# Kernel tuning notes

Measured on AMD Instinct MI355X. Metric: run time of the kernel, lower is better.

Reference implementation:

```python
import jax, jax.numpy as jnp
import numpy as np

N = 51200      # total nodes
E = 1638400    # total edges (avg degree 32)
G = 512        # graphs in batch
IN = 16        # input node features
H = 4          # heads
C = 32         # channels per head
HC = H * C     # 128, concat output width
SLOPE = 0.2    # LeakyReLU negative slope
BN_EPS = 1e-5


def _glorot(k, shape, fan):
    return jax.random.normal(k, shape, jnp.float32) / np.sqrt(fan).astype(np.float32)


def setup_inputs() -> dict:
    key = jax.random.key(0)
    ks = jax.random.split(key, 32)
    inp = {}
    inp['x'] = jax.random.normal(ks[0], (N, IN), jnp.float32)
    inp['edge_index'] = jax.random.randint(ks[1], (2, E), 0, N)
    inp['batch'] = jnp.sort(jax.random.randint(ks[2], (N,), 0, G))
    # GATv2 layer 1 (IN -> H*C)
    inp['l1_Wl'] = _glorot(ks[3], (IN, HC), IN)
    inp['l1_bl'] = jnp.zeros((HC,), jnp.float32)
    inp['l1_Wr'] = _glorot(ks[4], (IN, HC), IN)
    inp['l1_br'] = jnp.zeros((HC,), jnp.float32)
    inp['l1_att'] = _glorot(ks[5], (H, C), C)
    inp['l1_bias'] = jnp.zeros((HC,), jnp.float32)
    # GATv2 layer 2 (HC -> H*C)
    inp['l2_Wl'] = _glorot(ks[6], (HC, HC), HC)
    inp['l2_bl'] = jnp.zeros((HC,), jnp.float32)
    inp['l2_Wr'] = _glorot(ks[7], (HC, HC), HC)
    inp['l2_br'] = jnp.zeros((HC,), jnp.float32)
    inp['l2_att'] = _glorot(ks[8], (H, C), C)
    inp['l2_bias'] = jnp.zeros((HC,), jnp.float32)
    # MLP head (HC -> HC -> HC -> 2) with BatchNorm (eval mode, running stats 0/1)
    inp['fc1_W'] = _glorot(ks[9], (HC, HC), HC)
    inp['fc1_b'] = jnp.zeros((HC,), jnp.float32)
    inp['bn1_g'] = jnp.ones((HC,), jnp.float32)
    inp['bn1_b'] = jnp.zeros((HC,), jnp.float32)
    inp['fc2_W'] = _glorot(ks[10], (HC, HC), HC)
    inp['fc2_b'] = jnp.zeros((HC,), jnp.float32)
    inp['bn2_g'] = jnp.ones((HC,), jnp.float32)
    inp['bn2_b'] = jnp.zeros((HC,), jnp.float32)
    inp['fc3_W'] = _glorot(ks[11], (HC, 2), HC)
    inp['fc3_b'] = jnp.zeros((2,), jnp.float32)
    return inp


def gatv2_conv(x, src, dst, Wl, bl, Wr, br, att, bias):
    # PyG GATv2Conv (share_weights=False, concat=True), eval mode (no dropout).
    xl = (x @ Wl + bl).reshape(-1, H, C)  # source transform  [N,H,C]
    xr = (x @ Wr + br).reshape(-1, H, C)  # target transform  [N,H,C]
    e = jax.nn.leaky_relu(xl[src] + xr[dst], SLOPE)   # [E,H,C]
    score = jnp.einsum('ehc,hc->eh', e, att)          # [E,H]
    # segment softmax over edges sharing the same target node
    m = jax.ops.segment_max(score, dst, num_segments=N)
    ex = jnp.exp(score - m[dst])
    denom = jax.ops.segment_sum(ex, dst, num_segments=N)
    alpha = ex / (denom[dst] + 1e-16)                 # [E,H]
    out = jax.ops.segment_sum(xl[src] * alpha[:, :, None], dst, num_segments=N)
    return out.reshape(-1, HC) + bias


def reference(x, edge_index, batch,
              l1_Wl, l1_bl, l1_Wr, l1_br, l1_att, l1_bias,
              l2_Wl, l2_bl, l2_Wr, l2_br, l2_att, l2_bias,
              fc1_W, fc1_b, bn1_g, bn1_b,
              fc2_W, fc2_b, bn2_g, bn2_b,
              fc3_W, fc3_b):
    src, dst = edge_index[0], edge_index[1]
    h = jax.nn.relu(gatv2_conv(x, src, dst, l1_Wl, l1_bl, l1_Wr, l1_br, l1_att, l1_bias))
    h = jax.nn.relu(gatv2_conv(h, src, dst, l2_Wl, l2_bl, l2_Wr, l2_br, l2_att, l2_bias))
    # global mean pool over graphs
    s = jax.ops.segment_sum(h, batch, num_segments=G)
    cnt = jax.ops.segment_sum(jnp.ones((N,), h.dtype), batch, num_segments=G)
    g = s / jnp.maximum(cnt, 1.0)[:, None]            # [G,HC]
    # MLP head; BatchNorm1d in eval mode with running_mean=0, running_var=1
    def bn(z, gamma, beta):
        return z * (gamma / np.sqrt(1.0 + BN_EPS).astype(np.float32)) + beta
    g = jax.nn.relu(bn(g @ fc1_W + fc1_b, bn1_g, bn1_b))
    g = jax.nn.relu(bn(g @ fc2_W + fc2_b, bn2_g, bn2_b))
    return g @ fc3_W + fc3_b                          # [G,2]
```

## Files before the change

kernel.cpp:

```cpp
#include <hip/hip_runtime.h>
#include <math.h>

#define NN 51200
#define EE 1638400
#define GG 512
#define INF 16
#define HCC 128
#define NB 400
#define TILE 4096

typedef float vf2 __attribute__((ext_vector_type(2)));
#define FMA2 __builtin_elementwise_fma
#define MIN2 __builtin_elementwise_min
#define MAX2 __builtin_elementwise_max


__global__ __launch_bounds__(256) void k_hist(const int* __restrict__ ei,
                                              int* __restrict__ bcnt) {
    __shared__ int h[NB];
    for (int i = threadIdx.x; i < NB; i += 256) h[i] = 0;
    __syncthreads();
    int e0 = blockIdx.x * TILE;
#pragma unroll
    for (int s = 0; s < 16; s++) {
        int d = ei[EE + e0 + s * 256 + threadIdx.x];
        atomicAdd(&h[d >> 7], 1);
    }
    __syncthreads();
    for (int i = threadIdx.x; i < NB; i += 256)
        if (h[i]) atomicAdd(&bcnt[i], h[i]);
}

__global__ __launch_bounds__(512) void k_scan2(const int* __restrict__ bcnt,
                                               int* __restrict__ bbase,
                                               int* __restrict__ gcur,
                                               int* __restrict__ rowptr) {
    __shared__ int sc[512];
    int t = threadIdx.x;
    int v = (t < NB) ? bcnt[t] : 0;
    sc[t] = v;
    __syncthreads();
    for (int off = 1; off < 512; off <<= 1) {
        int u = (t >= off) ? sc[t - off] : 0;
        __syncthreads();
        sc[t] += u;
        __syncthreads();
    }
    if (t < NB) { int ex = sc[t] - v; bbase[t] = ex; gcur[t] = ex; }
    if (t == 0) { bbase[NB] = EE; rowptr[NN] = EE; }
}

__global__ __launch_bounds__(512) void k_bin(const int* __restrict__ ei,
                                             int* __restrict__ gcur,
                                             unsigned* __restrict__ binned) {
    __shared__ int h[512];
    __shared__ int lexcl[NB], lcur[NB], baseg[NB];
    __shared__ unsigned stage[TILE];
    int t = threadIdx.x;
    h[t] = 0;
    __syncthreads();
    int e0 = blockIdx.x * TILE;
    int sv[8], dv[8];
#pragma unroll
    for (int s = 0; s < 8; s++) {
        int e = e0 + s * 512 + t;
        sv[s] = ei[e];
        dv[s] = ei[EE + e];
        atomicAdd(&h[dv[s] >> 7], 1);
    }
    __syncthreads();
    int myh = h[t];
    for (int off = 1; off < 512; off <<= 1) {
        int u = (t >= off) ? h[t - off] : 0;
        __syncthreads();
        h[t] += u;
        __syncthreads();
    }
    if (t < NB) {
        int ex = h[t] - myh;
        lexcl[t] = ex;
        lcur[t] = ex;
        baseg[t] = atomicAdd(&gcur[t], myh);
    }
    __syncthreads();
#pragma unroll
    for (int s = 0; s < 8; s++) {
        int b = dv[s] >> 7;
        int r = atomicAdd(&lcur[b], 1);
        stage[r] = (unsigned)sv[s] | ((unsigned)dv[s] << 16);
    }
    __syncthreads();
#pragma unroll
    for (int s = 0; s < 8; s++) {
        int idx = s * 512 + t;
        unsigned p = stage[idx];
        int b = (int)(p >> 23);
        binned[baseg[b] + idx - lexcl[b]] = p;
    }
}

__global__ __launch_bounds__(256) void k_csr(const unsigned* __restrict__ binned,
                                             const int* __restrict__ bbase,
                                             int* __restrict__ rowptr,
                                             int* __restrict__ col) {
    int b = blockIdx.x;
    int base = bbase[b];
    int cnt = bbase[b + 1] - base;
    __shared__ int nh[128], ncur[128];
    int t = threadIdx.x;
    if (t < 128) nh[t] = 0;
    __syncthreads();
    for (int e = t; e < cnt; e += 256) {
        unsigned p = binned[base + e];
        atomicAdd(&nh[(p >> 16) & 127], 1);
    }
    __syncthreads();
    int myv = (t < 128) ? nh[t] : 0;
    for (int off = 1; off < 128; off <<= 1) {
        int u = (t >= off && t < 128) ? nh[t - off] : 0;
        __syncthreads();
        if (t < 128) nh[t] += u;
        __syncthreads();
    }
    if (t < 128) {
        int ex = nh[t] - myv;
        rowptr[(b << 7) + t] = base + ex;
        ncur[t] = base + ex;
    }
    __syncthreads();
    for (int e = t; e < cnt; e += 256) {
        unsigned p = binned[base + e];
        int r = atomicAdd(&ncur[(p >> 16) & 127], 1);
        col[r] = (int)(p & 0xFFFFu);
    }
}

__global__ __launch_bounds__(256) void k_lin1(const float* __restrict__ x,
                                              const float* __restrict__ Wl,
                                              const float* __restrict__ bl,
                                              const float* __restrict__ Wr,
                                              const float* __restrict__ br,
                                              float* __restrict__ xl,
                                              float* __restrict__ xr) {
    __shared__ float sx[2][INF];
    int j = threadIdx.x & 127;
    int ty = threadIdx.x >> 7;
    int row = blockIdx.x * 2 + ty;
    if (threadIdx.x < 32) {
        int r = blockIdx.x * 2 + (threadIdx.x >> 4);
        sx[threadIdx.x >> 4][threadIdx.x & 15] = x[(size_t)r * INF + (threadIdx.x & 15)];
    }
    __syncthreads();
    float al = bl[j], ar = br[j];
#pragma unroll
    for (int k = 0; k < INF; k++) {
        float xv = sx[ty][k];
        al = fmaf(xv, Wl[k * HCC + j], al);
        ar = fmaf(xv, Wr[k * HCC + j], ar);
    }
    int s = 64 * ((j >> 2) & 1) + 4 * (j >> 3) + (j & 3);
    xl[(size_t)row * HCC + s] = al;
    xr[(size_t)row * HCC + s] = ar;
}

#define AST 129
#define BST 260
__global__ __launch_bounds__(512) void k_lin2(const float* __restrict__ hin,
                                              const float* __restrict__ Wl,
                                              const float* __restrict__ bl,
                                              const float* __restrict__ Wr,
                                              const float* __restrict__ br,
                                              float* __restrict__ outl,
                                              float* __restrict__ outr) {
    __shared__ float As[32 * AST];
    __shared__ float Bs[32 * BST];
    const int tid = threadIdx.x;
    const int cx = tid & 31;
    const int cy = tid >> 5;
    const int r0 = blockIdx.x * 128;

    float accL[8][4], accR[8][4];
#pragma unroll
    for (int j = 0; j < 8; j++)
#pragma unroll
        for (int i = 0; i < 4; i++) { accL[j][i] = 0.f; accR[j][i] = 0.f; }

    for (int k0 = 0; k0 < HCC; k0 += 32) {
#pragma unroll
        for (int s = 0; s < 2; s++) {
            int f = tid + 512 * s;
            int row = f >> 3;
            int kk = (f & 7) * 4;
            float4 v = *(const float4*)(hin + (size_t)(r0 + row) * HCC + k0 + kk);
            As[(kk + 0) * AST + row] = v.x;
            As[(kk + 1) * AST + row] = v.y;
            As[(kk + 2) * AST + row] = v.z;
            As[(kk + 3) * AST + row] = v.w;
        }
#pragma unroll
        for (int s = 0; s < 4; s++) {
            int g = tid + 512 * s;
            int kr = g >> 6;
            int c4 = g & 63;
            const float* srcp = (c4 < 32)
                ? (Wl + (size_t)(k0 + kr) * HCC + c4 * 4)
                : (Wr + (size_t)(k0 + kr) * HCC + (c4 - 32) * 4);
            *(float4*)&Bs[kr * BST + c4 * 4] = *(const float4*)srcp;
        }
        __syncthreads();
#pragma unroll 4
        for (int k = 0; k < 32; ++k) {
            float a[8];
#pragma unroll
            for (int j = 0; j < 8; ++j) a[j] = As[k * AST + cy + 16 * j];
            float4 b4l = *(const float4*)&Bs[k * BST + cx * 4];
            float4 b4r = *(const float4*)&Bs[k * BST + 128 + cx * 4];
#pragma unroll
            for (int j = 0; j < 8; ++j) {
                accL[j][0] = fmaf(a[j], b4l.x, accL[j][0]);
                accL[j][1] = fmaf(a[j], b4l.y, accL[j][1]);
                accL[j][2] = fmaf(a[j], b4l.z, accL[j][2]);
                accL[j][3] = fmaf(a[j], b4l.w, accL[j][3]);
                accR[j][0] = fmaf(a[j], b4r.x, accR[j][0]);
                accR[j][1] = fmaf(a[j], b4r.y, accR[j][1]);
                accR[j][2] = fmaf(a[j], b4r.z, accR[j][2]);
                accR[j][3] = fmaf(a[j], b4r.w, accR[j][3]);
            }
        }
        __syncthreads();
    }
    float4 bv_l = *(const float4*)(bl + cx * 4);
    float4 bv_r = *(const float4*)(br + cx * 4);
    const int soff = 64 * (cx & 1) + (cx >> 1) * 4;
#pragma unroll
    for (int j = 0; j < 8; ++j) {
        int row = r0 + cy + 16 * j;
        float4 o;
        o.x = accL[j][0] + bv_l.x;
        o.y = accL[j][1] + bv_l.y;
        o.z = accL[j][2] + bv_l.z;
        o.w = accL[j][3] + bv_l.w;
        *(float4*)(outl + (size_t)row * HCC + soff) = o;
        o.x = accR[j][0] + bv_r.x;
        o.y = accR[j][1] + bv_r.y;
        o.z = accR[j][2] + bv_r.z;
        o.w = accR[j][3] + bv_r.w;
        *(float4*)(outr + (size_t)row * HCC + soff) = o;
    }
}

__global__ __launch_bounds__(256) void k_attn(const int* __restrict__ rowptr,
                                              const int* __restrict__ col,
                                              const float* __restrict__ xl,
                                              const float* __restrict__ xr,
                                              const float* __restrict__ att,
                                              const float* __restrict__ bias,
                                              float* __restrict__ hout) {
    const int wave = threadIdx.x >> 6;
    const int lane = threadIdx.x & 63;
    const int sub = lane >> 4;
    const int q = lane & 15;
    const int n = blockIdx.x * 4 + wave;

    const float4 xrv0 = *(const float4*)(xr + (size_t)n * HCC + q * 4);
    const float4 xrv1 = *(const float4*)(xr + (size_t)n * HCC + 64 + q * 4);
    const float4 at0 = *(const float4*)(att + q * 8);
    const float4 at1 = *(const float4*)(att + q * 8 + 4);
    const vf2 xr01 = {xrv0.x, xrv0.y}, xr23 = {xrv0.z, xrv0.w};
    const vf2 xr45 = {xrv1.x, xrv1.y}, xr67 = {xrv1.z, xrv1.w};
    const vf2 at01 = {at0.x, at0.y}, at23 = {at0.z, at0.w};
    const vf2 at45 = {at1.x, at1.y}, at67 = {at1.z, at1.w};
    const vf2 Z2 = {0.f, 0.f}, C2 = {0.2f, 0.2f};
    const unsigned choff = (unsigned)q * 16u;

    const int base = rowptr[n];
    const int deg = rowptr[n + 1] - base;

    float m = -INFINITY, l = 0.f;
    vf2 a01 = Z2, a23 = Z2, a45 = Z2, a67 = Z2;

    for (int i0 = 0; i0 < deg; i0 += 64) {
        int mye = 0;
        if (i0 + lane < deg) mye = col[base + i0 + lane];
        const int cnt = min(64, deg - i0);
        const int groups = (cnt + 15) >> 4;
        for (int g = 0; g < groups; ++g) {
            vf2 v01[4], v23[4], v45[4], v67[4];
#pragma unroll
            for (int k = 0; k < 4; ++k) {
                const int src = __shfl(mye, 16 * g + 4 * k + sub);
                const unsigned voff = ((unsigned)src << 9) + choff;
                const float4 v0 = *(const float4*)((const char*)xl + voff);
                const float4 v1 = *(const float4*)((const char*)xl + voff + 256);
                v01[k] = (vf2){v0.x, v0.y}; v23[k] = (vf2){v0.z, v0.w};
                v45[k] = (vf2){v1.x, v1.y}; v67[k] = (vf2){v1.z, v1.w};
            }
            float p[4];
#pragma unroll
            for (int k = 0; k < 4; ++k) {
                vf2 e, kk, p2;
                e = v01[k] + xr01; kk = FMA2(C2, MIN2(e, Z2), MAX2(e, Z2)); p2 = kk * at01;
                e = v23[k] + xr23; kk = FMA2(C2, MIN2(e, Z2), MAX2(e, Z2)); p2 = FMA2(kk, at23, p2);
                e = v45[k] + xr45; kk = FMA2(C2, MIN2(e, Z2), MAX2(e, Z2)); p2 = FMA2(kk, at45, p2);
                e = v67[k] + xr67; kk = FMA2(C2, MIN2(e, Z2), MAX2(e, Z2)); p2 = FMA2(kk, at67, p2);
                float pp = p2.x + p2.y;
                pp += __shfl_xor(pp, 1);
                pp += __shfl_xor(pp, 2);
                if ((16 * g + 4 * k + sub) >= cnt) pp = -INFINITY;
                p[k] = pp;
            }
            float pm = fmaxf(fmaxf(p[0], p[1]), fmaxf(p[2], p[3]));
            pm = fmaxf(pm, __shfl_xor(pm, 16));
            pm = fmaxf(pm, __shfl_xor(pm, 32));
            const float mn = fmaxf(m, pm);
            const float sc = __expf(m - mn);
            const float w0 = __expf(p[0] - mn);
            const float w1 = __expf(p[1] - mn);
            const float w2 = __expf(p[2] - mn);
            const float w3 = __expf(p[3] - mn);
            l = fmaf(l, sc, (w0 + w1) + (w2 + w3));
            const vf2 S = {sc, sc};
            const vf2 W0 = {w0, w0}, W1 = {w1, w1}, W2 = {w2, w2}, W3 = {w3, w3};
            a01 = FMA2(W3, v01[3], FMA2(W2, v01[2], FMA2(W1, v01[1], FMA2(W0, v01[0], a01 * S))));
            a23 = FMA2(W3, v23[3], FMA2(W2, v23[2], FMA2(W1, v23[1], FMA2(W0, v23[0], a23 * S))));
            a45 = FMA2(W3, v45[3], FMA2(W2, v45[2], FMA2(W1, v45[1], FMA2(W0, v45[0], a45 * S))));
            a67 = FMA2(W3, v67[3], FMA2(W2, v67[2], FMA2(W1, v67[1], FMA2(W0, v67[0], a67 * S))));
            m = mn;
        }
    }
    l += __shfl_xor(l, 16);
    l += __shfl_xor(l, 32);
    float af[8] = {a01.x, a01.y, a23.x, a23.y, a45.x, a45.y, a67.x, a67.y};
#pragma unroll
    for (int i = 0; i < 8; i++) {
        af[i] += __shfl_xor(af[i], 16);
        af[i] += __shfl_xor(af[i], 32);
    }
    const float inv = 1.f / (l + 1e-16f);
    if (sub == 0) {
        const float4 b0 = *(const float4*)(bias + q * 8);
        const float4 b1 = *(const float4*)(bias + q * 8 + 4);
        float4 o0, o1;
        o0.x = fmaxf(fmaf(af[0], inv, b0.x), 0.f);
        o0.y = fmaxf(fmaf(af[1], inv, b0.y), 0.f);
        o0.z = fmaxf(fmaf(af[2], inv, b0.z), 0.f);
        o0.w = fmaxf(fmaf(af[3], inv, b0.w), 0.f);
        o1.x = fmaxf(fmaf(af[4], inv, b1.x), 0.f);
        o1.y = fmaxf(fmaf(af[5], inv, b1.y), 0.f);
        o1.z = fmaxf(fmaf(af[6], inv, b1.z), 0.f);
        o1.w = fmaxf(fmaf(af[7], inv, b1.w), 0.f);
        *(float4*)(hout + (size_t)n * HCC + q * 8) = o0;
        *(float4*)(hout + (size_t)n * HCC + q * 8 + 4) = o1;
    }
}

__global__ __launch_bounds__(128) void k_head(const float* __restrict__ h,
                                              const int* __restrict__ batch,
                                              const float* __restrict__ fc1W, const float* __restrict__ fc1b,
                                              const float* __restrict__ bn1g, const float* __restrict__ bn1b,
                                              const float* __restrict__ fc2W, const float* __restrict__ fc2b,
                                              const float* __restrict__ bn2g, const float* __restrict__ bn2b,
                                              const float* __restrict__ fc3W, const float* __restrict__ fc3b,
                                              float* __restrict__ out) {
    int g = blockIdx.x;
    int j = threadIdx.x;
    __shared__ float buf[HCC], buf2[HCC];
    int lo = 0, hi = NN;
    while (lo < hi) { int mid = (lo + hi) >> 1; if (batch[mid] < g) lo = mid + 1; else hi = mid; }
    int s = lo;
    lo = 0; hi = NN;
    while (lo < hi) { int mid = (lo + hi) >> 1; if (batch[mid] < g + 1) lo = mid + 1; else hi = mid; }
    int e = lo;
    float sum = 0.f;
    for (int n = s; n < e; n++) sum += h[(size_t)n * HCC + j];
    float cnt = (float)(e - s);
    buf[j] = sum / fmaxf(cnt, 1.0f);
    __syncthreads();
    const float SQ = 1.00000499998749994f;
    float a = fc1b[j];
    for (int k = 0; k < HCC; k++) a = fmaf(buf[k], fc1W[k * HCC + j], a);
    a = fmaf(a, bn1g[j] / SQ, bn1b[j]);
    a = fmaxf(a, 0.f);
    buf2[j] = a;
    __syncthreads();
    a = fc2b[j];
    for (int k = 0; k < HCC; k++) a = fmaf(buf2[k], fc2W[k * HCC + j], a);
    a = fmaf(a, bn2g[j] / SQ, bn2b[j]);
    a = fmaxf(a, 0.f);
    buf[j] = a;
    __syncthreads();
    if (j < 2) {
        float o = fc3b[j];
        for (int k = 0; k < HCC; k++) o = fmaf(buf[k], fc3W[k * 2 + j], o);
        out[g * 2 + j] = o;
    }
}

extern "C" void kernel_launch(void* const* d_in, const int* in_sizes, int n_in,
                              void* d_out, int out_size, void* d_ws, size_t ws_size,
                              hipStream_t stream) {
    const float* x      = (const float*)d_in[0];
    const int*   ei     = (const int*)d_in[1];
    const int*   batch  = (const int*)d_in[2];
    const float* l1_Wl  = (const float*)d_in[3];
    const float* l1_bl  = (const float*)d_in[4];
    const float* l1_Wr  = (const float*)d_in[5];
    const float* l1_br  = (const float*)d_in[6];
    const float* l1_att = (const float*)d_in[7];
    const float* l1_bias= (const float*)d_in[8];
    const float* l2_Wl  = (const float*)d_in[9];
    const float* l2_bl  = (const float*)d_in[10];
    const float* l2_Wr  = (const float*)d_in[11];
    const float* l2_br  = (const float*)d_in[12];
    const float* l2_att = (const float*)d_in[13];
    const float* l2_bias= (const float*)d_in[14];
    const float* fc1_W  = (const float*)d_in[15];
    const float* fc1_b  = (const float*)d_in[16];
    const float* bn1_g  = (const float*)d_in[17];
    const float* bn1_b  = (const float*)d_in[18];
    const float* fc2_W  = (const float*)d_in[19];
    const float* fc2_b  = (const float*)d_in[20];
    const float* bn2_g  = (const float*)d_in[21];
    const float* bn2_b  = (const float*)d_in[22];
    const float* fc3_W  = (const float*)d_in[23];
    const float* fc3_b  = (const float*)d_in[24];
    float* out = (float*)d_out;

    float* xl = (float*)d_ws;
    float* xr = xl + (size_t)NN * HCC;
    float* h  = xr + (size_t)NN * HCC;
    int* rowptr = (int*)(h + (size_t)NN * HCC);
    int* col    = rowptr + (NN + 1);
    int* bcnt   = col + EE;
    int* bbase  = bcnt + NB;
    int* gcur   = bbase + (NB + 1);
    unsigned* binned = (unsigned*)xl;

    hipMemsetAsync(bcnt, 0, NB * sizeof(int), stream);
    k_hist<<<EE / TILE, 256, 0, stream>>>(ei, bcnt);
    k_scan2<<<1, 512, 0, stream>>>(bcnt, bbase, gcur, rowptr);
    k_bin<<<EE / TILE, 512, 0, stream>>>(ei, gcur, binned);
    k_csr<<<NB, 256, 0, stream>>>(binned, bbase, rowptr, col);

    k_lin1<<<NN / 2, 256, 0, stream>>>(x, l1_Wl, l1_bl, l1_Wr, l1_br, xl, xr);
    k_attn<<<NN / 4, 256, 0, stream>>>(rowptr, col, xl, xr, l1_att, l1_bias, h);

    k_lin2<<<NN / 128, 512, 0, stream>>>(h, l2_Wl, l2_bl, l2_Wr, l2_br, xl, xr);
    k_attn<<<NN / 4, 256, 0, stream>>>(rowptr, col, xl, xr, l2_att, l2_bias, h);

    k_head<<<GG, 128, 0, stream>>>(h, batch, fc1_W, fc1_b, bn1_g, bn1_b,
                                   fc2_W, fc2_b, bn2_g, bn2_b, fc3_W, fc3_b, out);
}
```

Before: 516.4 us.

## Sort CSR columns by source bucket and use wave-shuffle scans

The CSR build now partitions each destination row's edges into 8 buckets keyed by the top bits of the source index, so neighbor lists are roughly ordered by source. The aim is better cache locality for the later xl[src] gathers. The shared-memory Hillis-Steele scans in k_bin and k_csr are replaced by wave shuffle scans with per-wave sums, which cuts barrier count. The pooling loop in k_head is split into four accumulators for more memory-level parallelism, which changes the order of float summation.

```diff
diff --git a/kernel.cpp b/kernel.cpp
--- a/kernel.cpp
+++ b/kernel.cpp
@@ -14,6 +14,15 @@
 #define MIN2 __builtin_elementwise_min
 #define MAX2 __builtin_elementwise_max
 
+
+__device__ __forceinline__ int wave_incl_scan(int v, int lane) {
+#pragma unroll
+    for (int d = 1; d < 64; d <<= 1) {
+        int y = __shfl_up(v, d);
+        if (lane >= d) v += y;
+    }
+    return v;
+}
 
 __global__ __launch_bounds__(256) void k_hist(const int* __restrict__ ei,
                                               int* __restrict__ bcnt) {
@@ -56,7 +65,9 @@
     __shared__ int h[512];
     __shared__ int lexcl[NB], lcur[NB], baseg[NB];
     __shared__ unsigned stage[TILE];
+    __shared__ int wsum[8];
     int t = threadIdx.x;
+    int lane = t & 63, w = t >> 6;
     h[t] = 0;
     __syncthreads();
     int e0 = blockIdx.x * TILE;
@@ -70,14 +81,14 @@
     }
     __syncthreads();
     int myh = h[t];
-    for (int off = 1; off < 512; off <<= 1) {
-        int u = (t >= off) ? h[t - off] : 0;
-        __syncthreads();
-        h[t] += u;
-        __syncthreads();
-    }
+    int incl = wave_incl_scan(myh, lane);
+    if (lane == 63) wsum[w] = incl;
+    __syncthreads();
+    int woff = 0;
+    for (int i = 0; i < w; i++) woff += wsum[i];
+    incl += woff;
     if (t < NB) {
-        int ex = h[t] - myh;
+        int ex = incl - myh;
         lexcl[t] = ex;
         lcur[t] = ex;
         baseg[t] = atomicAdd(&gcur[t], myh);
@@ -106,32 +117,40 @@
     int b = blockIdx.x;
     int base = bbase[b];
     int cnt = bbase[b + 1] - base;
-    __shared__ int nh[128], ncur[128];
+    __shared__ int nh[1024], ncur[1024];
+    __shared__ int wsum[4];
     int t = threadIdx.x;
-    if (t < 128) nh[t] = 0;
+    int lane = t & 63, w = t >> 6;
+#pragma unroll
+    for (int i = 0; i < 4; i++) nh[t + 256 * i] = 0;
     __syncthreads();
     for (int e = t; e < cnt; e += 256) {
         unsigned p = binned[base + e];
-        atomicAdd(&nh[(p >> 16) & 127], 1);
-    }
-    __syncthreads();
-    int myv = (t < 128) ? nh[t] : 0;
-    for (int off = 1; off < 128; off <<= 1) {
-        int u = (t >= off && t < 128) ? nh[t - off] : 0;
-        __syncthreads();
-        if (t < 128) nh[t] += u;
-        __syncthreads();
-    }
-    if (t < 128) {
-        int ex = nh[t] - myv;
-        rowptr[(b << 7) + t] = base + ex;
-        ncur[t] = base + ex;
-    }
+        unsigned src = p & 0xFFFFu;
+        int key = (int)(((p >> 16) & 127u) << 3) | (int)(src >> 13);
+        atomicAdd(&nh[key], 1);
+    }
+    __syncthreads();
+    int c0 = nh[4 * t + 0], c1 = nh[4 * t + 1], c2 = nh[4 * t + 2], c3 = nh[4 * t + 3];
+    int tot = ((c0 + c1) + (c2 + c3));
+    int incl = wave_incl_scan(tot, lane);
+    if (lane == 63) wsum[w] = incl;
+    __syncthreads();
+    int woff = 0;
+    for (int i = 0; i < w; i++) woff += wsum[i];
+    int tex = incl + woff - tot;
+    ncur[4 * t + 0] = base + tex;
+    ncur[4 * t + 1] = base + tex + c0;
+    ncur[4 * t + 2] = base + tex + c0 + c1;
+    ncur[4 * t + 3] = base + tex + c0 + c1 + c2;
+    if ((t & 1) == 0) rowptr[(b << 7) + (t >> 1)] = base + tex;
     __syncthreads();
     for (int e = t; e < cnt; e += 256) {
         unsigned p = binned[base + e];
-        int r = atomicAdd(&ncur[(p >> 16) & 127], 1);
-        col[r] = (int)(p & 0xFFFFu);
+        unsigned src = p & 0xFFFFu;
+        int key = (int)(((p >> 16) & 127u) << 3) | (int)(src >> 13);
+        int r = atomicAdd(&ncur[key], 1);
+        col[r] = (int)src;
     }
 }
 
@@ -371,8 +390,16 @@
     lo = 0; hi = NN;
     while (lo < hi) { int mid = (lo + hi) >> 1; if (batch[mid] < g + 1) lo = mid + 1; else hi = mid; }
     int e = lo;
-    float sum = 0.f;
-    for (int n = s; n < e; n++) sum += h[(size_t)n * HCC + j];
+    float s0 = 0.f, s1 = 0.f, s2 = 0.f, s3 = 0.f;
+    int n = s;
+    for (; n + 3 < e; n += 4) {
+        s0 += h[(size_t)n * HCC + j];
+        s1 += h[(size_t)(n + 1) * HCC + j];
+        s2 += h[(size_t)(n + 2) * HCC + j];
+        s3 += h[(size_t)(n + 3) * HCC + j];
+    }
+    for (; n < e; n++) s0 += h[(size_t)n * HCC + j];
+    float sum = (s0 + s1) + (s2 + s3);
     float cnt = (float)(e - s);
     buf[j] = sum / fmaxf(cnt, 1.0f);
     __syncthreads();
```

Measured after the change: 490.5 us. 5.0% less time.
